# Kernel tuning notes

Hardware: AMD Instinct MI355X
Metric: run time of the kernel (lower is better)

## Reference

```python
import jax, jax.numpy as jnp
import numpy as np

T, S, B, E, H = 1024, 1024, 4, 1024, 16
D = E // H
SCALE = D ** -0.5


def setup_inputs() -> dict:
    key = jax.random.key(0)
    ks = jax.random.split(key, 10)
    std = 0.02
    return {
        "q": jax.random.normal(ks[0], (T, B, E), jnp.float32),
        "k": jax.random.normal(ks[1], (S, B, E), jnp.float32),
        "v": jax.random.normal(ks[2], (S, B, E), jnp.float32),
        "Wq": jax.random.normal(ks[3], (E, E), jnp.float32) * std,
        "Wk": jax.random.normal(ks[4], (E, E), jnp.float32) * std,
        "Wv": jax.random.normal(ks[5], (E, E), jnp.float32) * std,
        "Wp": jax.random.normal(ks[6], (E, E), jnp.float32) * std,
        "bp": jnp.zeros((E,), jnp.float32),
        "attn_bias": jax.random.normal(ks[7], (B, H, T, S), jnp.float32) * std,
        "key_padding_mask": jax.random.bernoulli(ks[8], 0.1, (B, S)),
    }


def reference(q, k, v, Wq, Wk, Wv, Wp, bp, attn_bias, key_padding_mask):
    # projections (no bias: qkv_bias=False); torch Linear is x @ W.T
    qh = (q @ Wq.T).reshape(T, B, H, D).transpose(1, 2, 0, 3) * SCALE  # [B,H,T,D]
    kh = (k @ Wk.T).reshape(S, B, H, D).transpose(1, 2, 0, 3)          # [B,H,S,D]
    vh = (v @ Wv.T).reshape(S, B, H, D).transpose(1, 2, 0, 3)          # [B,H,S,D]

    scores = jnp.einsum("bhid,bhjd->bhij", qh, kh) + attn_bias        # [B,H,T,S]
    # detached max-subtract (as in original)
    scores = scores - jax.lax.stop_gradient(scores.max(axis=-1, keepdims=True))

    mask = key_padding_mask[:, None, None, :]                          # [B,1,1,S], True = masked
    neg = jnp.finfo(scores.dtype).min
    attn = jax.nn.softmax(jnp.where(mask, neg, scores), axis=-1)
    attn = jnp.where(mask, jnp.zeros((), scores.dtype), attn)          # XSoftmax: zero masked probs

    out = jnp.einsum("bhij,bhjd->bhid", attn, vh)                      # [B,H,T,D]
    out = out.transpose(2, 0, 1, 3).reshape(T, B, E)                   # [T,B,E]
    out = out @ Wp.T + bp                                              # output projection
    return (out, attn)
```

## Files before the change

kernel.cpp:

```cpp
#include <hip/hip_runtime.h>
#include <math.h>

constexpr int T_ = 1024, S_ = 1024, B_ = 4, E_ = 1024, H_ = 16, D_ = 64;
constexpr float SCALE_ = 0.125f;
constexpr size_t NH_ = (size_t)B_ * H_ * T_ * D_;
constexpr size_t EE_ = (size_t)E_ * E_;

typedef _Float16 h8 __attribute__((ext_vector_type(8)));
typedef _Float16 h4 __attribute__((ext_vector_type(4)));
typedef float f4 __attribute__((ext_vector_type(4)));

__device__ inline f4 mfma16(h8 a, h8 b, f4 c) {
    return __builtin_amdgcn_mfma_f32_16x16x32_f16(a, b, c, 0, 0, 0);
}

__device__ inline void gload_lds16(const void* g, void* l) {
    __builtin_amdgcn_global_load_lds(
        (const __attribute__((address_space(1))) void*)g,
        (__attribute__((address_space(3))) void*)l, 16, 0, 0);
}

__global__ __launch_bounds__(256) void cvt_all(
    const float* __restrict__ q, const float* __restrict__ k,
    const float* __restrict__ v, const float* __restrict__ wq,
    const float* __restrict__ wk, const float* __restrict__ wv,
    const float* __restrict__ wp, _Float16* __restrict__ dst)
{
    const int i8 = blockIdx.x * 256 + threadIdx.x;
    constexpr int BIG = (int)(NH_ / 8);
    constexpr int WSZ = (int)(EE_ / 8);
    const float* src;
    int loc;
    if (i8 < 3 * BIG) {
        int t = i8 / BIG; loc = i8 - t * BIG;
        src = t == 0 ? q : (t == 1 ? k : v);
    } else {
        int r = i8 - 3 * BIG;
        int t = r / WSZ; loc = r - t * WSZ;
        src = t == 0 ? wq : (t == 1 ? wk : (t == 2 ? wv : wp));
    }
    const float* p = src + (size_t)loc * 8;
    float4 a = *(const float4*)p;
    float4 b = *(const float4*)(p + 4);
    h8 o;
    o[0] = (_Float16)a.x; o[1] = (_Float16)a.y;
    o[2] = (_Float16)a.z; o[3] = (_Float16)a.w;
    o[4] = (_Float16)b.x; o[5] = (_Float16)b.y;
    o[6] = (_Float16)b.z; o[7] = (_Float16)b.w;
    *(h8*)&dst[(size_t)i8 * 8] = o;
}

template <typename EPI>
__device__ inline void gemm_core(
    const _Float16* __restrict__ A, const _Float16* __restrict__ W,
    int m0, int n0, EPI epi)
{
    __shared__ _Float16 As[64][64];
    __shared__ _Float16 Bs[128][64];

    const int tid = threadIdx.x;
    const int w = tid >> 6, l = tid & 63, lr = l & 15, lg = l >> 4;
    const int wr = w >> 2, wc = w & 3;

    const int srow = (w << 3) + (l >> 3);
    const int sg   = (l & 7) ^ (srow & 7);
    char* AsB = (char*)As;
    char* BsB = (char*)Bs;
    char* ldsA  = AsB + w * 1024;
    char* ldsB0 = BsB + w * 1024;
    char* ldsB1 = BsB + 8192 + w * 1024;

    f4 acc[2][2];
#pragma unroll
    for (int mi = 0; mi < 2; ++mi)
#pragma unroll
        for (int ni = 0; ni < 2; ++ni) acc[mi][ni] = (f4){0.f, 0.f, 0.f, 0.f};

    for (int k0 = 0; k0 < 1024; k0 += 64) {
        gload_lds16(&A[(size_t)(m0 + srow) * 1024 + k0 + sg * 8], ldsA);
        gload_lds16(&W[(size_t)(n0 + srow) * 1024 + k0 + sg * 8], ldsB0);
        gload_lds16(&W[(size_t)(n0 + 64 + srow) * 1024 + k0 + sg * 8], ldsB1);
        __syncthreads();
#pragma unroll
        for (int kk = 0; kk < 2; ++kk) {
            h8 af[2], bf[2];
#pragma unroll
            for (int mi = 0; mi < 2; ++mi) {
                int r = wr * 32 + mi * 16 + lr, kc = kk * 4 + lg;
                af[mi] = *(const h8*)(AsB + r * 128 + ((kc ^ (r & 7)) << 4));
            }
#pragma unroll
            for (int ni = 0; ni < 2; ++ni) {
                int r = wc * 32 + ni * 16 + lr, kc = kk * 4 + lg;
                bf[ni] = *(const h8*)(BsB + r * 128 + ((kc ^ (r & 7)) << 4));
            }
#pragma unroll
            for (int mi = 0; mi < 2; ++mi)
#pragma unroll
                for (int ni = 0; ni < 2; ++ni)
                    acc[mi][ni] = mfma16(af[mi], bf[ni], acc[mi][ni]);
        }
        __syncthreads();
    }

#pragma unroll
    for (int mi = 0; mi < 2; ++mi)
#pragma unroll
        for (int ni = 0; ni < 2; ++ni)
#pragma unroll
            for (int r = 0; r < 4; ++r) {
                int row = m0 + wr * 32 + mi * 16 + lg * 4 + r;
                int col = n0 + wc * 32 + ni * 16 + lr;
                epi(row, col, acc[mi][ni][r]);
            }
}

__global__ __launch_bounds__(512) void qkv_gemm(
    const _Float16* __restrict__ q16, const _Float16* __restrict__ k16,
    const _Float16* __restrict__ v16, const _Float16* __restrict__ Wq16,
    const _Float16* __restrict__ Wk16, const _Float16* __restrict__ Wv16,
    _Float16* __restrict__ qh, _Float16* __restrict__ kh,
    _Float16* __restrict__ vhT)
{
    const int z = blockIdx.z;
    const _Float16* A = z == 0 ? q16 : (z == 1 ? k16 : v16);
    const _Float16* W = z == 0 ? Wq16 : (z == 1 ? Wk16 : Wv16);
    _Float16* C = z == 0 ? qh : (z == 1 ? kh : vhT);
    const float scale = (z == 0) ? SCALE_ : 1.0f;
    const int m0 = blockIdx.x * 64, n0 = blockIdx.y * 128;

    if (z < 2) {
        gemm_core(A, W, m0, n0, [&](int row, int col, float vv) {
            int t = row >> 2, b = row & 3, h = col >> 6, d = col & 63;
            C[(((size_t)b * H_ + h) * T_ + t) * D_ + d] = (_Float16)(vv * scale);
        });
    } else {
        gemm_core(A, W, m0, n0, [&](int row, int col, float vv) {
            int s = row >> 2, b = row & 3, h = col >> 6, d = col & 63;
            C[(((size_t)b * H_ + h) * D_ + d) * S_ + s] = (_Float16)vv;
        });
    }
}

__global__ __launch_bounds__(512) void out_gemm(
    const _Float16* __restrict__ oh, const _Float16* __restrict__ Wp16,
    const float* __restrict__ bp, float* __restrict__ out)
{
    const int m0 = blockIdx.x * 64, n0 = blockIdx.y * 128;
    gemm_core(oh, Wp16, m0, n0, [&](int row, int col, float vv) {
        out[(size_t)row * E_ + col] = vv + bp[col];
    });
}

__global__ __launch_bounds__(512, 6) void fused_attn(
    const _Float16* __restrict__ qh, const _Float16* __restrict__ kh,
    const _Float16* __restrict__ vhT, const float* __restrict__ bias,
    const int* __restrict__ mask, float* __restrict__ attn,
    _Float16* __restrict__ oh)
{
    __shared__ _Float16 Pf[16 * 1024];
    __shared__ int aux_i[1024];
    __shared__ float wsum[8][16];
    __shared__ float sinv16[16];
    char* Pb = (char*)Pf;

    const int bid = blockIdx.x;
    const int vid = (bid & 7) * 512 + (bid >> 3);
    const int bh = vid >> 6;
    const int t0 = (vid & 63) * 16;
    const int b = bh >> 4, h = bh & 15;
    const int tid = threadIdx.x;
    const int w = tid >> 6, l = tid & 63, lr = l & 15, lg = l >> 4;

    const float* bbase = bias + ((size_t)bh * T_ + t0) * S_;
    const int brow_ = l >> 2, bq_ = l & 3;
    f4 bv[8];
#pragma unroll
    for (int j = 0; j < 8; ++j)
        bv[j] = *(const f4*)&bbase[(size_t)brow_ * S_ + w * 128 + j * 16 + bq_ * 4];

    const _Float16* qbase = qh + ((size_t)bh * T_ + t0) * D_;
    h8 qf0 = *(const h8*)&qbase[(size_t)lr * D_ + lg * 8];
    h8 qf1 = *(const h8*)&qbase[(size_t)lr * D_ + 32 + lg * 8];
    __builtin_amdgcn_sched_barrier(0);

    for (int i = tid; i < S_; i += 512) aux_i[i] = mask[(size_t)b * S_ + i];
    __syncthreads();

    const _Float16* kbase = kh + (size_t)bh * S_ * D_;
    const int wbase = w * 128;
    const int srcLane = lr * 4 + lg;

    float rs = 0.f;
#pragma unroll
    for (int sub = 0; sub < 8; ++sub) {
        int s0 = wbase + sub * 16;
        h8 kf0 = *(const h8*)&kbase[(size_t)(s0 + lr) * D_ + lg * 8];
        h8 kf1 = *(const h8*)&kbase[(size_t)(s0 + lr) * D_ + 32 + lg * 8];
        f4 c = (f4){0.f, 0.f, 0.f, 0.f};
        c = mfma16(kf0, qf0, c);
        c = mfma16(kf1, qf1, c);
        float b0 = __shfl(bv[sub][0], srcLane);
        float b1 = __shfl(bv[sub][1], srcLane);
        float b2 = __shfl(bv[sub][2], srcLane);
        float b3 = __shfl(bv[sub][3], srcLane);
        int4 mv = *(const int4*)&aux_i[s0 + lg * 4];
        float p0 = mv.x ? 0.f : __expf(c[0] + b0);
        float p1 = mv.y ? 0.f : __expf(c[1] + b1);
        float p2 = mv.z ? 0.f : __expf(c[2] + b2);
        float p3 = mv.w ? 0.f : __expf(c[3] + b3);
        rs += (p0 + p1) + (p2 + p3);
        h4 pv;
        pv[0] = (_Float16)p0; pv[1] = (_Float16)p1;
        pv[2] = (_Float16)p2; pv[3] = (_Float16)p3;
        int off = (lr * 2048 + (s0 + lg * 4) * 2) ^ ((lr & 7) << 4);
        *(h4*)(Pb + off) = pv;
    }
    rs += __shfl_xor(rs, 16); rs += __shfl_xor(rs, 32);
    if (l < 16) wsum[w][lr] = rs;
    __syncthreads();

    {
        const int rr2 = tid >> 5;
        const int c2  = tid & 31;
        float s8 = 0.f;
#pragma unroll
        for (int ww = 0; ww < 8; ++ww) s8 += wsum[ww][rr2];
        float inv = 1.0f / s8;
        if (c2 == 0) sinv16[rr2] = inv;
        float* arow = attn + ((size_t)bh * T_ + t0 + rr2) * S_;
#pragma unroll
        for (int j = 0; j < 8; ++j) {
            int col = c2 * 4 + j * 128;
            int off = (rr2 * 2048 + col * 2) ^ ((rr2 & 7) << 4);
            h4 p = *(const h4*)(Pb + off);
            f4 o = {(float)p[0] * inv, (float)p[1] * inv,
                    (float)p[2] * inv, (float)p[3] * inv};
            __builtin_nontemporal_store(o, (f4*)&arow[col]);
        }
    }

    {
        const int sh = w & 1, dbase = (w >> 1) * 16;
        const _Float16* vbase = vhT + (size_t)bh * D_ * S_;
        f4 acc = (f4){0.f, 0.f, 0.f, 0.f};
#pragma unroll 8
        for (int kc = 0; kc < 16; ++kc) {
            int s0 = sh * 512 + kc * 32;
            int off = (lr * 2048 + (s0 + lg * 8) * 2) ^ ((lr & 7) << 4);
            h8 pf = *(const h8*)(Pb + off);
            h8 vf = *(const h8*)&vbase[(size_t)(dbase + lr) * S_ + s0 + lg * 8];
            acc = mfma16(pf, vf, acc);
        }
        float* pvred = (float*)aux_i;
        if (sh) {
#pragma unroll
            for (int r = 0; r < 4; ++r)
                pvred[(lg * 4 + r) * 64 + dbase + lr] = acc[r];
        }
        __syncthreads();
        if (!sh) {
#pragma unroll
            for (int r = 0; r < 4; ++r) {
                int t = lg * 4 + r;
                float o = (acc[r] + pvred[t * 64 + dbase + lr]) * sinv16[t];
                oh[((size_t)(t0 + t) * B_ + b) * E_ + h * 64 + dbase + lr] = (_Float16)o;
            }
        }
    }
}

extern "C" void kernel_launch(void* const* d_in, const int* in_sizes, int n_in,
                              void* d_out, int out_size, void* d_ws, size_t ws_size,
                              hipStream_t stream)
{
    const float* q    = (const float*)d_in[0];
    const float* k    = (const float*)d_in[1];
    const float* v    = (const float*)d_in[2];
    const float* Wq   = (const float*)d_in[3];
    const float* Wk   = (const float*)d_in[4];
    const float* Wv   = (const float*)d_in[5];
    const float* Wp   = (const float*)d_in[6];
    const float* bp   = (const float*)d_in[7];
    const float* bias = (const float*)d_in[8];
    const int*   mask = (const int*)d_in[9];

    float* out  = (float*)d_out;
    float* attn = out + (size_t)T_ * B_ * E_;

    _Float16* qh   = (_Float16*)d_ws;
    _Float16* kh   = qh + NH_;
    _Float16* vhT  = kh + NH_;
    _Float16* oh   = vhT + NH_;
    _Float16* q16  = oh + NH_;
    _Float16* k16  = q16 + NH_;
    _Float16* v16  = k16 + NH_;
    _Float16* Wq16 = v16 + NH_;
    _Float16* Wk16 = Wq16 + EE_;
    _Float16* Wv16 = Wk16 + EE_;
    _Float16* Wp16 = Wv16 + EE_;

    dim3 blk(512);

    cvt_all<<<dim3(8192), dim3(256), 0, stream>>>(q, k, v, Wq, Wk, Wv, Wp, q16);

    qkv_gemm<<<dim3(64, 8, 3), blk, 0, stream>>>(
        q16, k16, v16, Wq16, Wk16, Wv16, qh, kh, vhT);

    fused_attn<<<dim3(4096), blk, 0, stream>>>(qh, kh, vhT, bias, mask, attn, oh);

    out_gemm<<<dim3(64, 8), blk, 0, stream>>>(oh, Wp16, bp, out);
}
```

Before: 259.3 us.

## Keep softmax probs in registers, store attn from MFMA layout, normalize before PV

Each lane now loads the bias directly in the MFMA output layout, so the cross-lane shuffles are gone. Unnormalized probabilities stay in registers until the row sum is known. They are then normalized, written to global attn straight from registers, and written to LDS in fp16 already scaled, so the later PV output needs no rescale. This removes the separate LDS readback pass for the attn store, but adds an extra barrier and more live registers, so the occupancy hint is lowered from 6 to 4. The attn global stores now come out as 16-byte chunks per lane spread over 16 rows, rather than row-contiguous per warp, which may hurt coalescing.

```diff
diff --git a/kernel.cpp b/kernel.cpp
--- a/kernel.cpp
+++ b/kernel.cpp
@@ -152,7 +152,7 @@
     });
 }
 
-__global__ __launch_bounds__(512, 6) void fused_attn(
+__global__ __launch_bounds__(512, 4) void fused_attn(
     const _Float16* __restrict__ qh, const _Float16* __restrict__ kh,
     const _Float16* __restrict__ vhT, const float* __restrict__ bias,
     const int* __restrict__ mask, float* __restrict__ attn,
@@ -161,7 +161,6 @@
     __shared__ _Float16 Pf[16 * 1024];
     __shared__ int aux_i[1024];
     __shared__ float wsum[8][16];
-    __shared__ float sinv16[16];
     char* Pb = (char*)Pf;
 
     const int bid = blockIdx.x;
@@ -171,26 +170,28 @@
     const int b = bh >> 4, h = bh & 15;
     const int tid = threadIdx.x;
     const int w = tid >> 6, l = tid & 63, lr = l & 15, lg = l >> 4;
-
-    const float* bbase = bias + ((size_t)bh * T_ + t0) * S_;
-    const int brow_ = l >> 2, bq_ = l & 3;
+    const int wbase = w * 128;
+
+    const float* brow = bias + ((size_t)bh * T_ + t0 + lr) * S_ + wbase + lg * 4;
     f4 bv[8];
 #pragma unroll
     for (int j = 0; j < 8; ++j)
-        bv[j] = *(const f4*)&bbase[(size_t)brow_ * S_ + w * 128 + j * 16 + bq_ * 4];
+        bv[j] = *(const f4*)&brow[j * 16];
 
     const _Float16* qbase = qh + ((size_t)bh * T_ + t0) * D_;
     h8 qf0 = *(const h8*)&qbase[(size_t)lr * D_ + lg * 8];
     h8 qf1 = *(const h8*)&qbase[(size_t)lr * D_ + 32 + lg * 8];
-    __builtin_amdgcn_sched_barrier(0);
 
     for (int i = tid; i < S_; i += 512) aux_i[i] = mask[(size_t)b * S_ + i];
+
+    asm volatile("" :: "v"(bv[0]), "v"(bv[1]), "v"(bv[2]), "v"(bv[3]),
+                       "v"(bv[4]), "v"(bv[5]), "v"(bv[6]), "v"(bv[7]),
+                       "v"(qf0), "v"(qf1));
     __syncthreads();
 
     const _Float16* kbase = kh + (size_t)bh * S_ * D_;
-    const int wbase = w * 128;
-    const int srcLane = lr * 4 + lg;
-
+
+    f4 p[8];
     float rs = 0.f;
 #pragma unroll
     for (int sub = 0; sub < 8; ++sub) {
@@ -200,45 +201,37 @@
         f4 c = (f4){0.f, 0.f, 0.f, 0.f};
         c = mfma16(kf0, qf0, c);
         c = mfma16(kf1, qf1, c);
-        float b0 = __shfl(bv[sub][0], srcLane);
-        float b1 = __shfl(bv[sub][1], srcLane);
-        float b2 = __shfl(bv[sub][2], srcLane);
-        float b3 = __shfl(bv[sub][3], srcLane);
         int4 mv = *(const int4*)&aux_i[s0 + lg * 4];
-        float p0 = mv.x ? 0.f : __expf(c[0] + b0);
-        float p1 = mv.y ? 0.f : __expf(c[1] + b1);
-        float p2 = mv.z ? 0.f : __expf(c[2] + b2);
-        float p3 = mv.w ? 0.f : __expf(c[3] + b3);
-        rs += (p0 + p1) + (p2 + p3);
-        h4 pv;
-        pv[0] = (_Float16)p0; pv[1] = (_Float16)p1;
-        pv[2] = (_Float16)p2; pv[3] = (_Float16)p3;
-        int off = (lr * 2048 + (s0 + lg * 4) * 2) ^ ((lr & 7) << 4);
-        *(h4*)(Pb + off) = pv;
+        f4 pj;
+        pj[0] = mv.x ? 0.f : __expf(c[0] + bv[sub][0]);
+        pj[1] = mv.y ? 0.f : __expf(c[1] + bv[sub][1]);
+        pj[2] = mv.z ? 0.f : __expf(c[2] + bv[sub][2]);
+        pj[3] = mv.w ? 0.f : __expf(c[3] + bv[sub][3]);
+        rs += (pj[0] + pj[1]) + (pj[2] + pj[3]);
+        p[sub] = pj;
     }
     rs += __shfl_xor(rs, 16); rs += __shfl_xor(rs, 32);
     if (l < 16) wsum[w][lr] = rs;
     __syncthreads();
 
-    {
-        const int rr2 = tid >> 5;
-        const int c2  = tid & 31;
-        float s8 = 0.f;
-#pragma unroll
-        for (int ww = 0; ww < 8; ++ww) s8 += wsum[ww][rr2];
-        float inv = 1.0f / s8;
-        if (c2 == 0) sinv16[rr2] = inv;
-        float* arow = attn + ((size_t)bh * T_ + t0 + rr2) * S_;
-#pragma unroll
-        for (int j = 0; j < 8; ++j) {
-            int col = c2 * 4 + j * 128;
-            int off = (rr2 * 2048 + col * 2) ^ ((rr2 & 7) << 4);
-            h4 p = *(const h4*)(Pb + off);
-            f4 o = {(float)p[0] * inv, (float)p[1] * inv,
-                    (float)p[2] * inv, (float)p[3] * inv};
-            __builtin_nontemporal_store(o, (f4*)&arow[col]);
-        }
-    }
+    float s8 = 0.f;
+#pragma unroll
+    for (int ww = 0; ww < 8; ++ww) s8 += wsum[ww][lr];
+    const float inv = 1.0f / s8;
+
+    float* arow = attn + ((size_t)bh * T_ + t0 + lr) * S_ + wbase + lg * 4;
+#pragma unroll
+    for (int sub = 0; sub < 8; ++sub) {
+        f4 o = {p[sub][0] * inv, p[sub][1] * inv,
+                p[sub][2] * inv, p[sub][3] * inv};
+        __builtin_nontemporal_store(o, (f4*)&arow[sub * 16]);
+        h4 pn;
+        pn[0] = (_Float16)o[0]; pn[1] = (_Float16)o[1];
+        pn[2] = (_Float16)o[2]; pn[3] = (_Float16)o[3];
+        int off = (lr * 2048 + (wbase + sub * 16 + lg * 4) * 2) ^ ((lr & 7) << 4);
+        *(h4*)(Pb + off) = pn;
+    }
+    __syncthreads();
 
     {
         const int sh = w & 1, dbase = (w >> 1) * 16;
@@ -263,7 +256,7 @@
 #pragma unroll
             for (int r = 0; r < 4; ++r) {
                 int t = lg * 4 + r;
-                float o = (acc[r] + pvred[t * 64 + dbase + lr]) * sinv16[t];
+                float o = acc[r] + pvred[t * 64 + dbase + lr];
                 oh[((size_t)(t0 + t) * B_ + b) * E_ + h * 64 + dbase + lr] = (_Float16)o;
             }
         }
```

After: 290.9 us. 1.12x slower.
